# Performance work log

Measured on AMD Instinct MI355X. Metric: run time of the kernel, lower is better.

Reference implementation:

```python
import jax, jax.numpy as jnp
import numpy as np

M, N, DIM = 256, 256, 512
EPOCHS = 100
ALPHA = 0.3
RADIUS = 128.0


def setup_inputs() -> dict:
    key = jax.random.key(0)
    k1, k2 = jax.random.split(key)
    x = jax.random.normal(k1, (DIM,), dtype=jnp.float32)
    weights = jax.random.normal(k2, (M * N, DIM), dtype=jnp.float32)
    it = 10  # current training iteration (python int scalar)
    return {"x": x, "weights": weights, "it": it}


def reference(x, weights, it):
    # Squared L2 distance from x to every codebook/weight vector: [m*n]
    d2 = jnp.sum((x[None, :] - weights) ** 2, axis=1)
    bmu = jnp.argmin(d2)  # best matching unit index (scalar int)

    # Decayed learning rate and neighbourhood radius
    lr_decay = 1.0 - it / EPOCHS
    alpha_op = ALPHA * lr_decay
    radius_op = RADIUS * lr_decay

    # Grid locations, matching the original's (i // m, i % n) convention
    idx = jnp.arange(M * N)
    loc = jnp.stack([idx // M, idx % N], axis=1).astype(jnp.float32)  # [m*n, 2]
    bmu_loc = jnp.stack([bmu // M, bmu % N]).astype(jnp.float32)      # [2]

    # Squared grid distance to BMU and Gaussian neighbourhood function
    bmu_d2 = jnp.sum((bmu_loc[None, :] - loc) ** 2, axis=1)  # [m*n]
    neigh = jnp.exp(-bmu_d2 / (2.0 * radius_op ** 2))
    lr_op = alpha_op * neigh  # [m*n]

    # Neighbourhood-weighted pull of each weight vector toward x
    delta = lr_op[:, None] * (x[None, :] - weights)  # [m*n, dim]
    return weights + delta
```

## Files before the change

### kernel.cpp

```cpp
#include <hip/hip_runtime.h>
#include <hip/hip_bf16.h>
#include <math.h>

#define SOM_M 256
#define SOM_N 256
#define SOM_DIM 512
#define NROWS (SOM_M * SOM_N)
#define EPOCHS 100.0f
#define ALPHA 0.3f
#define RADIUS 128.0f

#define DIST_BLOCKS 1024

__global__ __launch_bounds__(256) void som_dist(
    const float* __restrict__ x, const float* __restrict__ w,
    float* __restrict__ pval, int* __restrict__ pidx) {
    __shared__ float xs[SOM_DIM];
    for (int j = threadIdx.x; j < SOM_DIM; j += 256) xs[j] = x[j];
    __syncthreads();

    const int wave = threadIdx.x >> 6;
    const int lane = threadIdx.x & 63;
    const int gwave = blockIdx.x * 4 + wave;
    const float4* xs4 = (const float4*)xs;
    const float4 xa = xs4[lane];
    const float4 xb = xs4[lane + 64];

    float best = INFINITY;
    int bidx = 0x7fffffff;

    for (int row = gwave; row < NROWS; row += DIST_BLOCKS * 4) {
        const float4* wr = (const float4*)(w + (size_t)row * SOM_DIM);
        float4 a = wr[lane];
        float4 b = wr[lane + 64];
        float t, d = 0.0f;
        t = a.x - xa.x; d += t * t;
        t = a.y - xa.y; d += t * t;
        t = a.z - xa.z; d += t * t;
        t = a.w - xa.w; d += t * t;
        t = b.x - xb.x; d += t * t;
        t = b.y - xb.y; d += t * t;
        t = b.z - xb.z; d += t * t;
        t = b.w - xb.w; d += t * t;
        #pragma unroll
        for (int s = 1; s < 64; s <<= 1) d += __shfl_xor(d, s);
        if (d < best) { best = d; bidx = row; }
    }

    __shared__ float bv[4];
    __shared__ int   bi[4];
    if (lane == 0) { bv[wave] = best; bi[wave] = bidx; }
    __syncthreads();
    if (threadIdx.x == 0) {
        float v = bv[0]; int i = bi[0];
        #pragma unroll
        for (int k = 1; k < 4; ++k) {
            if (bv[k] < v || (bv[k] == v && bi[k] < i)) { v = bv[k]; i = bi[k]; }
        }
        pval[blockIdx.x] = v;
        pidx[blockIdx.x] = i;
    }
}

__global__ __launch_bounds__(256) void som_argmin(
    const float* __restrict__ pval, const int* __restrict__ pidx,
    int* __restrict__ bmu_out) {
    __shared__ float sv[256];
    __shared__ int   si[256];
    float v = INFINITY; int idx = 0x7fffffff;
    for (int k = threadIdx.x; k < DIST_BLOCKS; k += 256) {
        float pv = pval[k]; int pi = pidx[k];
        if (pv < v || (pv == v && pi < idx)) { v = pv; idx = pi; }
    }
    sv[threadIdx.x] = v; si[threadIdx.x] = idx;
    __syncthreads();
    for (int s = 128; s > 0; s >>= 1) {
        if (threadIdx.x < s) {
            float ov = sv[threadIdx.x + s]; int oi = si[threadIdx.x + s];
            if (ov < sv[threadIdx.x] || (ov == sv[threadIdx.x] && oi < si[threadIdx.x])) {
                sv[threadIdx.x] = ov; si[threadIdx.x] = oi;
            }
        }
        __syncthreads();
    }
    if (threadIdx.x == 0) *bmu_out = si[0];
}

__global__ __launch_bounds__(256) void som_update(
    const float* __restrict__ x, const float* __restrict__ w,
    const int* __restrict__ it_ptr, const int* __restrict__ bmu_ptr,
    float* __restrict__ out) {
    const int bmu = *bmu_ptr;
    const float lr_decay = 1.0f - (float)(*it_ptr) / EPOCHS;
    const float alpha_op = ALPHA * lr_decay;
    const float radius_op = RADIUS * lr_decay;
    const float inv2r2 = 1.0f / (2.0f * radius_op * radius_op);

    const size_t tid = (size_t)blockIdx.x * 256 + threadIdx.x;
    const int row = (int)(tid >> 7);
    const int c4  = (int)(tid & 127);
    const int r = row >> 8, c = row & 255;
    const int br = bmu >> 8, bc = bmu & 255;
    const float dr = (float)(br - r), dc = (float)(bc - c);
    const float lr = alpha_op * expf(-(dr * dr + dc * dc) * inv2r2);

    const float4 wv = ((const float4*)w)[tid];
    const float4 xv = ((const float4*)x)[c4];
    float4 o;
    o.x = wv.x + lr * (xv.x - wv.x);
    o.y = wv.y + lr * (xv.y - wv.y);
    o.z = wv.z + lr * (xv.z - wv.z);
    o.w = wv.w + lr * (xv.w - wv.w);
    ((float4*)out)[tid] = o;
}

extern "C" void kernel_launch(void* const* d_in, const int* in_sizes, int n_in,
                              void* d_out, int out_size, void* d_ws, size_t ws_size,
                              hipStream_t stream) {
    const float* x = (const float*)d_in[0];
    const float* w = (const float*)d_in[1];
    const int* it  = (const int*)d_in[2];
    float* out = (float*)d_out;

    float* pval = (float*)d_ws;
    int*   pidx = (int*)((char*)d_ws + DIST_BLOCKS * sizeof(float));
    int*   bmu  = (int*)((char*)d_ws + 2 * DIST_BLOCKS * sizeof(float));

    som_dist<<<DIST_BLOCKS, 256, 0, stream>>>(x, w, pval, pidx);
    som_argmin<<<1, 256, 0, stream>>>(pval, pidx, bmu);

    const int total_f4 = NROWS * (SOM_DIM / 4);
    som_update<<<total_f4 / 256, 256, 0, stream>>>(x, w, it, bmu, out);
}
```

Before: 66.57 us.

## Fuse argmin into update kernel with packed 64-bit min keys and contiguous rows

Drops the single-block argmin kernel. Each of the 1024 update blocks now redundantly reduces the 1024 packed (distance bits, index) keys to find the BMU. The distance kernel switches to contiguous 64-row chunks per block, so the update blocks touch the same row ranges. The update kernel computes per-row learning rates once into shared memory and loops 32 float4 iterations per thread. This saves a kernel launch and the serial tiny reduction, at the cost of every update block rereading 8KB of partials.

```diff
diff --git a/kernel.cpp b/kernel.cpp
--- a/kernel.cpp
+++ b/kernel.cpp
@@ -6,30 +6,38 @@
 #define SOM_N 256
 #define SOM_DIM 512
 #define NROWS (SOM_M * SOM_N)
-#define EPOCHS 100.0f
-#define ALPHA 0.3f
-#define RADIUS 128.0f
 
-#define DIST_BLOCKS 1024
+#define GRID 1024
+#define BLOCK 256
+#define ROWS_PER_BLOCK (NROWS / GRID)
+#define F4_PER_ROW (SOM_DIM / 4)
+#define F4_PER_BLOCK (ROWS_PER_BLOCK * F4_PER_ROW)
+#define UPD_ITERS (F4_PER_BLOCK / BLOCK)
 
-__global__ __launch_bounds__(256) void som_dist(
+static __device__ __forceinline__ unsigned long long umin64(unsigned long long a,
+                                                            unsigned long long b) {
+    return a < b ? a : b;
+}
+
+__global__ __launch_bounds__(BLOCK) void som_dist(
     const float* __restrict__ x, const float* __restrict__ w,
-    float* __restrict__ pval, int* __restrict__ pidx) {
+    unsigned long long* __restrict__ ws) {
     __shared__ float xs[SOM_DIM];
-    for (int j = threadIdx.x; j < SOM_DIM; j += 256) xs[j] = x[j];
+    for (int j = threadIdx.x; j < SOM_DIM; j += BLOCK) xs[j] = x[j];
     __syncthreads();
 
     const int wave = threadIdx.x >> 6;
     const int lane = threadIdx.x & 63;
-    const int gwave = blockIdx.x * 4 + wave;
     const float4* xs4 = (const float4*)xs;
     const float4 xa = xs4[lane];
     const float4 xb = xs4[lane + 64];
 
     float best = INFINITY;
-    int bidx = 0x7fffffff;
-
-    for (int row = gwave; row < NROWS; row += DIST_BLOCKS * 4) {
+    int bidx = 0;
+    const int row0 = blockIdx.x * ROWS_PER_BLOCK + wave * 16;
+    #pragma unroll 2
+    for (int k = 0; k < 16; ++k) {
+        const int row = row0 + k;
         const float4* wr = (const float4*)(w + (size_t)row * SOM_DIM);
         float4 a = wr[lane];
         float4 b = wr[lane + 64];
@@ -47,71 +55,72 @@
         if (d < best) { best = d; bidx = row; }
     }
 
-    __shared__ float bv[4];
-    __shared__ int   bi[4];
-    if (lane == 0) { bv[wave] = best; bi[wave] = bidx; }
+    __shared__ unsigned long long sm[4];
+    if (lane == 0)
+        sm[wave] = ((unsigned long long)__float_as_uint(best) << 32) | (unsigned)bidx;
     __syncthreads();
     if (threadIdx.x == 0) {
-        float v = bv[0]; int i = bi[0];
+        unsigned long long m = sm[0];
         #pragma unroll
-        for (int k = 1; k < 4; ++k) {
-            if (bv[k] < v || (bv[k] == v && bi[k] < i)) { v = bv[k]; i = bi[k]; }
-        }
-        pval[blockIdx.x] = v;
-        pidx[blockIdx.x] = i;
+        for (int k = 1; k < 4; ++k) m = umin64(m, sm[k]);
+        ws[blockIdx.x] = m;
     }
 }
 
-__global__ __launch_bounds__(256) void som_argmin(
-    const float* __restrict__ pval, const int* __restrict__ pidx,
-    int* __restrict__ bmu_out) {
-    __shared__ float sv[256];
-    __shared__ int   si[256];
-    float v = INFINITY; int idx = 0x7fffffff;
-    for (int k = threadIdx.x; k < DIST_BLOCKS; k += 256) {
-        float pv = pval[k]; int pi = pidx[k];
-        if (pv < v || (pv == v && pi < idx)) { v = pv; idx = pi; }
+__global__ __launch_bounds__(BLOCK) void som_update(
+    const float* __restrict__ x, const float* __restrict__ w,
+    const int* __restrict__ it_ptr, const unsigned long long* __restrict__ ws,
+    float* __restrict__ out) {
+    __shared__ float xs[SOM_DIM];
+    __shared__ unsigned long long red[4];
+    __shared__ float lrs[ROWS_PER_BLOCK];
+
+    for (int j = threadIdx.x; j < SOM_DIM; j += BLOCK) xs[j] = x[j];
+
+    unsigned long long m = ws[threadIdx.x];
+    m = umin64(m, ws[threadIdx.x + 256]);
+    m = umin64(m, ws[threadIdx.x + 512]);
+    m = umin64(m, ws[threadIdx.x + 768]);
+    #pragma unroll
+    for (int s = 1; s < 64; s <<= 1) m = umin64(m, __shfl_xor(m, s));
+    const int wave = threadIdx.x >> 6;
+    const int lane = threadIdx.x & 63;
+    if (lane == 0) red[wave] = m;
+    __syncthreads();
+    if (threadIdx.x == 0) {
+        red[0] = umin64(umin64(red[0], red[1]), umin64(red[2], red[3]));
     }
-    sv[threadIdx.x] = v; si[threadIdx.x] = idx;
     __syncthreads();
-    for (int s = 128; s > 0; s >>= 1) {
-        if (threadIdx.x < s) {
-            float ov = sv[threadIdx.x + s]; int oi = si[threadIdx.x + s];
-            if (ov < sv[threadIdx.x] || (ov == sv[threadIdx.x] && oi < si[threadIdx.x])) {
-                sv[threadIdx.x] = ov; si[threadIdx.x] = oi;
-            }
-        }
-        __syncthreads();
+    const int bmu = (int)(red[0] & 0xFFFFFFFFull);
+
+    const float lr_decay = 1.0f - (float)(*it_ptr) * 0.01f;
+    const float alpha_op = 0.3f * lr_decay;
+    const float radius_op = 128.0f * lr_decay;
+    const float inv2r2 = 1.0f / (2.0f * radius_op * radius_op);
+    if (threadIdx.x < ROWS_PER_BLOCK) {
+        const int row = blockIdx.x * ROWS_PER_BLOCK + threadIdx.x;
+        const float dr = (float)((bmu >> 8) - (row >> 8));
+        const float dc = (float)((bmu & 255) - (row & 255));
+        lrs[threadIdx.x] = alpha_op * expf(-(dr * dr + dc * dc) * inv2r2);
     }
-    if (threadIdx.x == 0) *bmu_out = si[0];
-}
+    __syncthreads();
 
-__global__ __launch_bounds__(256) void som_update(
-    const float* __restrict__ x, const float* __restrict__ w,
-    const int* __restrict__ it_ptr, const int* __restrict__ bmu_ptr,
-    float* __restrict__ out) {
-    const int bmu = *bmu_ptr;
-    const float lr_decay = 1.0f - (float)(*it_ptr) / EPOCHS;
-    const float alpha_op = ALPHA * lr_decay;
-    const float radius_op = RADIUS * lr_decay;
-    const float inv2r2 = 1.0f / (2.0f * radius_op * radius_op);
-
-    const size_t tid = (size_t)blockIdx.x * 256 + threadIdx.x;
-    const int row = (int)(tid >> 7);
-    const int c4  = (int)(tid & 127);
-    const int r = row >> 8, c = row & 255;
-    const int br = bmu >> 8, bc = bmu & 255;
-    const float dr = (float)(br - r), dc = (float)(bc - c);
-    const float lr = alpha_op * expf(-(dr * dr + dc * dc) * inv2r2);
-
-    const float4 wv = ((const float4*)w)[tid];
-    const float4 xv = ((const float4*)x)[c4];
-    float4 o;
-    o.x = wv.x + lr * (xv.x - wv.x);
-    o.y = wv.y + lr * (xv.y - wv.y);
-    o.z = wv.z + lr * (xv.z - wv.z);
-    o.w = wv.w + lr * (xv.w - wv.w);
-    ((float4*)out)[tid] = o;
+    const float4* xs4 = (const float4*)xs;
+    const float4 xv = xs4[threadIdx.x & (F4_PER_ROW - 1)];
+    const size_t base = (size_t)blockIdx.x * F4_PER_BLOCK;
+    const int rsub = threadIdx.x >> 7;
+    #pragma unroll 4
+    for (int i = 0; i < UPD_ITERS; ++i) {
+        const size_t idx = base + (size_t)i * BLOCK + threadIdx.x;
+        const float lr = lrs[i * 2 + rsub];
+        const float4 wv = ((const float4*)w)[idx];
+        float4 o;
+        o.x = wv.x + lr * (xv.x - wv.x);
+        o.y = wv.y + lr * (xv.y - wv.y);
+        o.z = wv.z + lr * (xv.z - wv.z);
+        o.w = wv.w + lr * (xv.w - wv.w);
+        ((float4*)out)[idx] = o;
+    }
 }
 
 extern "C" void kernel_launch(void* const* d_in, const int* in_sizes, int n_in,
@@ -121,14 +130,8 @@
     const float* w = (const float*)d_in[1];
     const int* it  = (const int*)d_in[2];
     float* out = (float*)d_out;
+    unsigned long long* ws = (unsigned long long*)d_ws;
 
-    float* pval = (float*)d_ws;
-    int*   pidx = (int*)((char*)d_ws + DIST_BLOCKS * sizeof(float));
-    int*   bmu  = (int*)((char*)d_ws + 2 * DIST_BLOCKS * sizeof(float));
-
-    som_dist<<<DIST_BLOCKS, 256, 0, stream>>>(x, w, pval, pidx);
-    som_argmin<<<1, 256, 0, stream>>>(pval, pidx, bmu);
-
-    const int total_f4 = NROWS * (SOM_DIM / 4);
-    som_update<<<total_f4 / 256, 256, 0, stream>>>(x, w, it, bmu, out);
+    som_dist<<<GRID, BLOCK, 0, stream>>>(x, w, ws);
+    som_update<<<GRID, BLOCK, 0, stream>>>(x, w, it, ws, out);
 }
```

New measurement: 67.56 us. About the same (+1.5%).
